# Performance work log

Hardware: AMD Instinct MI355X
Metric: run time of the kernel (lower is better)

## Reference

```python
import jax, jax.numpy as jnp
import numpy as np

B, S, H = 2, 1024, 4096
NH, NKV, HD = 32, 8, 128
THETA = 500000.0
EPS = 1e-6


def _ste(x, q):
    # straight-through estimator: forward q, gradient of identity
    return x + jax.lax.stop_gradient(q - x)


def weight_quant(w):
    # BitNet b1.58 ternary weight quantization (per-tensor mean-abs scale)
    scale = 1.0 / jnp.clip(jnp.mean(jnp.abs(w)), 1e-5)
    wq = jnp.clip(jnp.round(w * scale), -1.0, 1.0) / scale
    return _ste(w, wq)


def act_quant(x):
    # per-token int8 absmax activation quantization
    scale = 127.0 / jnp.clip(jnp.max(jnp.abs(x), axis=-1, keepdims=True), 1e-5)
    xq = jnp.clip(jnp.round(x * scale), -128.0, 127.0) / scale
    return _ste(x, xq)


def bitlinear(x, w):
    # torch Linear convention: w is (out, in)
    return act_quant(x) @ weight_quant(w).T


def rmsnorm(x, w):
    return x * jax.lax.rsqrt(jnp.mean(x * x, axis=-1, keepdims=True) + EPS) * w


def rope(x, cos, sin):
    # x: (b, s, h, hd); pairs are interleaved (even, odd) like view_as_complex
    x2 = x.reshape(*x.shape[:-1], HD // 2, 2)
    a, b = x2[..., 0], x2[..., 1]
    c = cos[None, :, None, :]
    s = sin[None, :, None, :]
    out = jnp.stack([a * c - b * s, a * s + b * c], axis=-1)
    return out.reshape(x.shape)


def setup_inputs() -> dict:
    key = jax.random.key(0)
    ks = jax.random.split(key, 6)
    hidden_states = jax.random.normal(ks[0], (B, S, H), dtype=jnp.float32)
    causal = jnp.tril(jnp.ones((S, S), dtype=bool))
    attention_mask = jnp.where(causal, 0.0, -1e9).astype(jnp.float32)[None, None]
    w_q = jax.random.normal(ks[1], (NH * HD, H), dtype=jnp.float32) * 0.02
    w_k = jax.random.normal(ks[2], (NKV * HD, H), dtype=jnp.float32) * 0.02
    w_v = jax.random.normal(ks[3], (NKV * HD, H), dtype=jnp.float32) * 0.02
    w_o = jax.random.normal(ks[4], (H, NH * HD), dtype=jnp.float32) * 0.02
    subln_w = jnp.ones((NH * HD,), dtype=jnp.float32)
    return {"hidden_states": hidden_states, "attention_mask": attention_mask,
            "w_q": w_q, "w_k": w_k, "w_v": w_v, "w_o": w_o, "subln_w": subln_w}


def reference(hidden_states, attention_mask, w_q, w_k, w_v, w_o, subln_w):
    b, s, _ = hidden_states.shape
    # RoPE tables (precomputed buffer in torch, constant here)
    inv_freq = 1.0 / (THETA ** (jnp.arange(0, HD, 2, dtype=jnp.float32) / HD))
    freqs = jnp.arange(s, dtype=jnp.float32)[:, None] * inv_freq[None, :]  # (s, hd/2)
    cos, sin = jnp.cos(freqs), jnp.sin(freqs)

    q = bitlinear(hidden_states, w_q).reshape(b, s, NH, HD)
    k = bitlinear(hidden_states, w_k).reshape(b, s, NKV, HD)
    v = bitlinear(hidden_states, w_v).reshape(b, s, NKV, HD)

    q = rope(q, cos, sin)
    k = rope(k, cos, sin)

    # GQA: repeat kv heads
    n_rep = NH // NKV
    k = jnp.repeat(k, n_rep, axis=2)  # (b, s, NH, hd)
    v = jnp.repeat(v, n_rep, axis=2)

    scale = 1.0 / np.sqrt(HD)
    scores = jnp.einsum('bqhd,bkhd->bhqk', q, k) * scale
    scores = scores + attention_mask
    attn = jax.nn.softmax(scores.astype(jnp.float32), axis=-1).astype(q.dtype)
    out = jnp.einsum('bhqk,bkhd->bqhd', attn, v).reshape(b, s, NH * HD)

    out = rmsnorm(out, subln_w)  # SubLN before output projection
    out = bitlinear(out, w_o)
    return out
```

## Files before the change

kernel.cpp:

```cpp
#include <hip/hip_runtime.h>
#include <hip/hip_bf16.h>
#include <cstdint>

typedef unsigned short u16;
typedef __bf16 bf16x8 __attribute__((ext_vector_type(8)));
typedef float f32x4 __attribute__((ext_vector_type(4)));
typedef int i32x4 __attribute__((ext_vector_type(4)));

#define SEQ 1024
#define HID 4096
#define NHQ 32
#define NKVH 8
#define HDIM 128
#define NB 2
#define NROWS (NB*SEQ)

static __device__ __forceinline__ u16 f2bf(float x) {
  __hip_bfloat16 h = __float2bfloat16(x);
  return *reinterpret_cast<u16*>(&h);
}

static __device__ __forceinline__ void gload16(const void* g, void* l) {
  __builtin_amdgcn_global_load_lds((__attribute__((address_space(1))) void*)(void*)g,
                                   (__attribute__((address_space(3))) void*)l, 16, 0, 0);
}

static __device__ __forceinline__ int pack4i8(float a, float b, float c, float d,
                                              float s, float lo, float hi) {
  int x0 = (int)fminf(fmaxf(rintf(a*s), lo), hi);
  int x1 = (int)fminf(fmaxf(rintf(b*s), lo), hi);
  int x2 = (int)fminf(fmaxf(rintf(c*s), lo), hi);
  int x3 = (int)fminf(fmaxf(rintf(d*s), lo), hi);
  return (x0 & 255) | ((x1 & 255) << 8) | ((x2 & 255) << 16) | ((x3 & 255) << 24);
}

__global__ __launch_bounds__(256) void k_abssum4(const float* __restrict__ wq_, const float* __restrict__ wk_,
                                                 const float* __restrict__ wv_, const float* __restrict__ wo_,
                                                 float* __restrict__ partial) {
  int bx = blockIdx.x;
  const float* w; long n4; int pbase, lb, nb;
  if (bx < 1024)      { w = wq_; n4 = 4194304; pbase = 0;    lb = bx;        nb = 1024; }
  else if (bx < 1280) { w = wk_; n4 = 1048576; pbase = 1024; lb = bx - 1024; nb = 256; }
  else if (bx < 1536) { w = wv_; n4 = 1048576; pbase = 1280; lb = bx - 1280; nb = 256; }
  else                { w = wo_; n4 = 4194304; pbase = 1536; lb = bx - 1536; nb = 1024; }
  float s = 0.f;
  long stride = (long)nb * 256;
  const float4* w4 = (const float4*)w;
  for (long j = (long)lb*256 + threadIdx.x; j < n4; j += stride) {
    float4 v = w4[j];
    s += fabsf(v.x) + fabsf(v.y) + fabsf(v.z) + fabsf(v.w);
  }
  #pragma unroll
  for (int off = 1; off < 64; off <<= 1) s += __shfl_xor(s, off);
  __shared__ float red[4];
  if ((threadIdx.x & 63) == 0) red[threadIdx.x >> 6] = s;
  __syncthreads();
  if (threadIdx.x == 0) partial[pbase + lb] = red[0] + red[1] + red[2] + red[3];
}

__global__ __launch_bounds__(256) void k_wscale(const float* __restrict__ partial,
                                                float* __restrict__ wsc) {
  __shared__ float red[4];
  const float nelem[4] = {16777216.f, 4194304.f, 4194304.f, 16777216.f};
  const int pbase[4] = {0, 1024, 1280, 1536};
  const int pcnt[4]  = {1024, 256, 256, 1024};
  for (int wi = 0; wi < 4; ++wi) {
    float s = 0.f;
    for (int j = threadIdx.x; j < pcnt[wi]; j += 256) s += partial[pbase[wi] + j];
    #pragma unroll
    for (int off = 1; off < 64; off <<= 1) s += __shfl_xor(s, off);
    if ((threadIdx.x & 63) == 0) red[threadIdx.x >> 6] = s;
    __syncthreads();
    if (threadIdx.x == 0) wsc[wi] = fmaxf((red[0]+red[1]+red[2]+red[3]) / nelem[wi], 1e-5f);
    __syncthreads();
  }
}

__global__ __launch_bounds__(256) void k_quantw8_all(const float* __restrict__ wq_, const float* __restrict__ wk_,
                                                     const float* __restrict__ wv_, const float* __restrict__ wo_,
                                                     char* __restrict__ oq_, char* __restrict__ ok_,
                                                     char* __restrict__ ov_, char* __restrict__ oo_,
                                                     const float* __restrict__ wsc) {
  int bx = blockIdx.x;
  const float* src; char* dst; int idx; long base;
  if (bx < 16384)      { src = wq_; dst = oq_; idx = 0; base = bx; }
  else if (bx < 20480) { src = wk_; dst = ok_; idx = 1; base = bx - 16384; }
  else if (bx < 24576) { src = wv_; dst = ov_; idx = 2; base = bx - 20480; }
  else                 { src = wo_; dst = oo_; idx = 3; base = bx - 24576; }
  long j = base*256 + threadIdx.x;
  long oj = j;
  if (idx <= 1) {
    long row = j >> 10;
    int u = (int)(row & 31);
    long prow = (row & ~31L) | (long)((u >> 1) | ((u & 1) << 4));
    oj = (prow << 10) | (j & 1023);
  }
  float inv = 1.0f / wsc[idx];
  float4 v = ((const float4*)src)[j];
  ((int*)dst)[oj] = pack4i8(v.x, v.y, v.z, v.w, inv, -1.f, 1.f);
}

__global__ __launch_bounds__(256) void k_actq8(const float* __restrict__ x, char* __restrict__ xq,
                                               float* __restrict__ xs) {
  long row = blockIdx.x;
  const float4* xr = (const float4*)(x + row*HID);
  float4 v[4];
  float am = 0.f;
  #pragma unroll
  for (int j = 0; j < 4; ++j) {
    v[j] = xr[j*256 + threadIdx.x];
    am = fmaxf(am, fmaxf(fmaxf(fabsf(v[j].x), fabsf(v[j].y)), fmaxf(fabsf(v[j].z), fabsf(v[j].w))));
  }
  #pragma unroll
  for (int off = 1; off < 64; off <<= 1) am = fmaxf(am, __shfl_xor(am, off));
  __shared__ float red[4];
  if ((threadIdx.x & 63) == 0) red[threadIdx.x >> 6] = am;
  __syncthreads();
  am = fmaxf(fmaxf(red[0], red[1]), fmaxf(red[2], red[3]));
  float amc = fmaxf(am, 1e-5f);
  float s = 127.0f / amc;
  int* oq = (int*)(xq + row*HID);
  #pragma unroll
  for (int j = 0; j < 4; ++j)
    oq[j*256 + threadIdx.x] = pack4i8(v[j].x, v[j].y, v[j].z, v[j].w, s, -128.f, 127.f);
  if (threadIdx.x == 0) xs[row] = amc / 127.0f;
}

__global__ __launch_bounds__(256, 4) void k_gemm8(const char* __restrict__ A, const char* __restrict__ W,
                                                  float* __restrict__ C, const float* __restrict__ arow,
                                                  const float* __restrict__ wsc, int widx,
                                                  int M, int N, int K) {
  __shared__ char As[2][64*64] __attribute__((aligned(16)));
  __shared__ char Ws_[2][128*64] __attribute__((aligned(16)));
  int t = threadIdx.x;
  int l = (blockIdx.x & 7) * 128 + (blockIdx.x >> 3);
  int bn = l >> 5, bm = l & 31;
  const char* Ab = A + (long)bm*64*K;
  const char* Wb = W + (long)bn*128*K;
  int lane = t & 63, wid = t >> 6;
  int wr = wid >> 1, wc = wid & 1;
  int lrow = lane & 15, l8 = lane >> 4;
  int xsw = (lrow >> 1) & 3;
  int ch0 = (l8 ^ xsw) * 16;
  i32x4 zero = {0, 0, 0, 0};
  i32x4 acc[2][4];
  #pragma unroll
  for (int mi = 0; mi < 2; ++mi)
    #pragma unroll
    for (int ni = 0; ni < 4; ++ni) acc[mi][ni] = zero;

  int r0 = t >> 2;
  int c0 = ((t & 3) ^ ((t >> 3) & 3)) * 16;
  auto stage = [&](int buf, int kt) {
    gload16(Ab + (long)r0*K + kt*64 + c0, &As[buf][t*16]);
    gload16(Wb + (long)r0*K + kt*64 + c0, &Ws_[buf][t*16]);
    gload16(Wb + (long)(r0+64)*K + kt*64 + c0, &Ws_[buf][(t+256)*16]);
  };

  int nk = K >> 6;
  stage(0, 0);
  __syncthreads();
  int cur = 0;
  for (int kt = 0; kt < nk; ++kt) {
    if (kt + 1 < nk) stage(cur ^ 1, kt + 1);
    i32x4 af[2], bfr[4];
    #pragma unroll
    for (int mi = 0; mi < 2; ++mi) af[mi] = *(const i32x4*)&As[cur][(wr*32 + mi*16 + lrow)*64 + ch0];
    #pragma unroll
    for (int ni = 0; ni < 4; ++ni) bfr[ni] = *(const i32x4*)&Ws_[cur][(wc*64 + ni*16 + lrow)*64 + ch0];
    __builtin_amdgcn_s_setprio(1);
    #pragma unroll
    for (int mi = 0; mi < 2; ++mi)
      #pragma unroll
      for (int ni = 0; ni < 4; ++ni)
        acc[mi][ni] = __builtin_amdgcn_mfma_i32_16x16x64_i8(af[mi], bfr[ni], acc[mi][ni], 0, 0, 0);
    __builtin_amdgcn_s_setprio(0);
    __syncthreads();
    cur ^= 1;
  }
  float ws = wsc[widx];
  #pragma unroll
  for (int mi = 0; mi < 2; ++mi)
    #pragma unroll
    for (int r = 0; r < 4; ++r) {
      int row = bm*64 + wr*32 + mi*16 + l8*4 + r;
      float sc = arow[row] * ws;
      #pragma unroll
      for (int ni = 0; ni < 4; ++ni) {
        int col = bn*128 + wc*64 + ni*16 + lrow;
        C[(long)row*N + col] = (float)acc[mi][ni][r] * sc;
      }
    }
}

__global__ __launch_bounds__(256) void k_gemm8_qkv(const char* __restrict__ A,
    const char* __restrict__ Wq, const char* __restrict__ Wk, const char* __restrict__ Wv,
    u16* __restrict__ Qb, u16* __restrict__ Kb, u16* __restrict__ Vt,
    const float* __restrict__ arow, const float* __restrict__ wsc,
    const float* __restrict__ cosb, const float* __restrict__ sinb) {
  const int K = 4096;
  int bx = (blockIdx.x & 7) * 96 + (blockIdx.x >> 3);
  int kind, bm, bn;
  const char* W;
  if (bx < 512)      { kind = 0; bm = bx >> 5;          bn = bx & 31; W = Wq; }
  else if (bx < 640) { kind = 1; bm = (bx - 512) >> 3;  bn = bx & 7;  W = Wk; }
  else               { kind = 2; bm = (bx - 640) >> 3;  bn = bx & 7;  W = Wv; }

  __shared__ char As[2][128*64] __attribute__((aligned(16)));
  __shared__ char Ws_[2][128*64] __attribute__((aligned(16)));
  int t = threadIdx.x;
  const char* Ab = A + (long)bm*128*K;
  const char* Wb = W + (long)bn*128*K;
  int lane = t & 63, wid = t >> 6;
  int wr = wid >> 1, wc = wid & 1;
  int lrow = lane & 15, l8 = lane >> 4;
  int xsw = (lrow >> 1) & 3;
  int ch0 = (l8 ^ xsw) * 16;
  i32x4 zero = {0, 0, 0, 0};
  i32x4 acc[4][4];
  #pragma unroll
  for (int mi = 0; mi < 4; ++mi)
    #pragma unroll
    for (int ni = 0; ni < 4; ++ni) acc[mi][ni] = zero;

  int f0 = t, f1 = t + 256;
  int r0 = f0 >> 2, c0 = ((f0 & 3) ^ ((f0 >> 3) & 3)) * 16;
  int r1 = f1 >> 2;
  auto stage = [&](int buf, int kt) {
    gload16(Ab + (long)r0*K + kt*64 + c0, &As[buf][f0*16]);
    gload16(Ab + (long)r1*K + kt*64 + c0, &As[buf][f1*16]);
    gload16(Wb + (long)r0*K + kt*64 + c0, &Ws_[buf][f0*16]);
    gload16(Wb + (long)r1*K + kt*64 + c0, &Ws_[buf][f1*16]);
  };

  stage(0, 0);
  __syncthreads();
  int cur = 0;
  for (int kt = 0; kt < (K >> 6); ++kt) {
    if (kt + 1 < (K >> 6)) stage(cur ^ 1, kt + 1);
    i32x4 af[4], bfr[4];
    #pragma unroll
    for (int mi = 0; mi < 4; ++mi) af[mi] = *(const i32x4*)&As[cur][(wr*64 + mi*16 + lrow)*64 + ch0];
    #pragma unroll
    for (int ni = 0; ni < 4; ++ni) bfr[ni] = *(const i32x4*)&Ws_[cur][(wc*64 + ni*16 + lrow)*64 + ch0];
    __builtin_amdgcn_s_setprio(1);
    #pragma unroll
    for (int mi = 0; mi < 4; ++mi)
      #pragma unroll
      for (int ni = 0; ni < 4; ++ni)
        acc[mi][ni] = __builtin_amdgcn_mfma_i32_16x16x64_i8(af[mi], bfr[ni], acc[mi][ni], 0, 0, 0);
    __builtin_amdgcn_s_setprio(0);
    __syncthreads();
    cur ^= 1;
  }

  if (kind == 2) {
    float ws = wsc[2];
    #pragma unroll
    for (int mi = 0; mi < 4; ++mi) {
      int row0 = bm*128 + wr*64 + mi*16 + l8*4;
      int bidx = row0 >> 10, s0 = row0 & 1023;
      #pragma unroll
      for (int ni = 0; ni < 4; ++ni) {
        int col = bn*128 + wc*64 + ni*16 + lrow;
        int hkv = col >> 7, d = col & 127;
        ushort4 o4;
        o4.x = f2bf((float)acc[mi][ni][0] * arow[row0+0] * ws);
        o4.y = f2bf((float)acc[mi][ni][1] * arow[row0+1] * ws);
        o4.z = f2bf((float)acc[mi][ni][2] * arow[row0+2] * ws);
        o4.w = f2bf((float)acc[mi][ni][3] * arow[row0+3] * ws);
        *(ushort4*)&Vt[(((long)bidx*NKVH + hkv)*HDIM + d)*SEQ + s0] = o4;
      }
    }
  } else {
    float ws = wsc[kind];
    u16* dst = kind ? Kb : Qb;
    int nh = kind ? NKVH : NHQ;
    #pragma unroll
    for (int mi = 0; mi < 4; ++mi) {
      #pragma unroll
      for (int r = 0; r < 4; ++r) {
        int row = bm*128 + wr*64 + mi*16 + l8*4 + r;
        int bidx = row >> 10, s = row & 1023;
        float sc = arow[row] * ws;
        #pragma unroll
        for (int j = 0; j < 2; ++j) {
          float a  = (float)acc[mi][2*j][r] * sc;
          float b2 = (float)acc[mi][2*j+1][r] * sc;
          int B = bn*128 + wc*64 + j*32;
          int h = B >> 7;
          int d = (B & 127) + 2*lrow;
          int i = d >> 1;
          float cc = cosb[(s << 6) + i], sn = sinb[(s << 6) + i];
          ushort2 o2;
          o2.x = f2bf(a*cc - b2*sn);
          o2.y = f2bf(a*sn + b2*cc);
          *(ushort2*)&dst[(((long)bidx*nh + h)*SEQ + s)*HDIM + d] = o2;
        }
      }
    }
  }
}

__global__ __launch_bounds__(256) void k_ropetab(float* __restrict__ cosb, float* __restrict__ sinb) {
  int idx = blockIdx.x*256 + threadIdx.x;
  int s = idx >> 6, i = idx & 63;
  float e = (2.0f * (float)i) / 128.0f;
  float inv = 1.0f / powf(500000.0f, e);
  float f = (float)s * inv;
  cosb[idx] = cosf(f);
  sinb[idx] = sinf(f);
}

__global__ __launch_bounds__(256) void k_attn(const u16* __restrict__ qb, const u16* __restrict__ kb,
                                              const u16* __restrict__ vt, float* __restrict__ ao) {
  int p = blockIdx.x, h = blockIdx.y, b = blockIdx.z;
  int t = threadIdx.x, lane = t & 63, wid = t >> 6;
  int lrow = lane & 15, l8 = lane >> 4;
  int x7 = lrow & 7;

  __shared__ u16 Ks[2][64*128] __attribute__((aligned(16)));
  __shared__ u16 Vs[2][128*64] __attribute__((aligned(16)));
  __shared__ u16 Ps[4][16][72] __attribute__((aligned(16)));

  const u16* kp = kb + ((long)(b*NKVH + (h >> 2)))*SEQ*HDIM;
  const u16* vp = vt + ((long)(b*NKVH + (h >> 2)))*HDIM*SEQ;

  auto stageK = [&](int buf, int j) {
    const u16* src = kp + (long)j*64*HDIM;
    #pragma unroll
    for (int i = 0; i < 4; ++i) {
      int r0 = wid*16 + i*4;
      int row = r0 + (lane >> 4);
      int cg = (lane & 15) ^ (row & 7);
      gload16(src + (long)row*HDIM + cg*8, &Ks[buf][r0*HDIM]);
    }
  };
  auto stageV = [&](int buf, int j) {
    #pragma unroll
    for (int i = 0; i < 4; ++i) {
      int r0 = wid*32 + i*8;
      int row = r0 + (lane >> 3);
      int cg = (lane & 7) ^ (row & 7);
      gload16(vp + (long)row*SEQ + j*64 + cg*8, &Vs[buf][r0*64]);
    }
  };

  for (int phase = 0; phase < 2; ++phase) {
    int qt = phase ? (15 - p) : p;
    int q0 = qt*64 + wid*16;
    const u16* qp = qb + (((long)(b*NHQ + h))*SEQ + q0)*HDIM;
    bf16x8 qf[4];
    #pragma unroll
    for (int ks = 0; ks < 4; ++ks) qf[ks] = *(const bf16x8*)&qp[lrow*HDIM + ks*32 + l8*8];
    f32x4 zero = {0.f, 0.f, 0.f, 0.f};
    f32x4 o[8];
    #pragma unroll
    for (int f = 0; f < 8; ++f) o[f] = zero;
    float m[4], ll[4];
    #pragma unroll
    for (int r = 0; r < 4; ++r) { m[r] = -1e30f; ll[r] = 0.f; }

    int nj = qt + 1;
    stageK(0, 0); stageV(0, 0);
    __syncthreads();
    int cur = 0;
    for (int j = 0; j < nj; ++j) {
      if (j + 1 < nj) { stageK(cur ^ 1, j + 1); stageV(cur ^ 1, j + 1); }
      const u16* Kc = Ks[cur];
      const u16* Vc = Vs[cur];
      f32x4 sc4[4];
      #pragma unroll
      for (int ni = 0; ni < 4; ++ni) sc4[ni] = zero;
      __builtin_amdgcn_s_setprio(1);
      #pragma unroll
      for (int ni = 0; ni < 4; ++ni) {
        int row = ni*16 + lrow;
        #pragma unroll
        for (int ks = 0; ks < 4; ++ks) {
          int cl = (ks*4 + l8) ^ x7;
          bf16x8 kfr = *(const bf16x8*)&Kc[row*HDIM + cl*8];
          sc4[ni] = __builtin_amdgcn_mfma_f32_16x16x32_bf16(qf[ks], kfr, sc4[ni], 0, 0, 0);
        }
      }
      __builtin_amdgcn_s_setprio(0);
      const float scale = 0.08838834764831845f;
      float pm[4] = {-1e30f, -1e30f, -1e30f, -1e30f};
      float pv[4][4];
      bool diag = (j == qt);
      #pragma unroll
      for (int ni = 0; ni < 4; ++ni) {
        int kv = j*64 + ni*16 + lrow;
        #pragma unroll
        for (int r = 0; r < 4; ++r) {
          int qr = q0 + l8*4 + r;
          float val = sc4[ni][r] * scale;
          if (diag && kv > qr) val = -1e30f;
          pv[ni][r] = val;
          pm[r] = fmaxf(pm[r], val);
        }
      }
      #pragma unroll
      for (int r = 0; r < 4; ++r) {
        #pragma unroll
        for (int off = 1; off < 16; off <<= 1) pm[r] = fmaxf(pm[r], __shfl_xor(pm[r], off));
      }
      float fr[4], rs[4];
      #pragma unroll
      for (int r = 0; r < 4; ++r) {
        float nm = fmaxf(m[r], pm[r]);
        fr[r] = __expf(m[r] - nm);
        m[r] = nm; rs[r] = 0.f;
      }
      #pragma unroll
      for (int ni = 0; ni < 4; ++ni)
        #pragma unroll
        for (int r = 0; r < 4; ++r) {
          float pe = __expf(pv[ni][r] - m[r]);
          pv[ni][r] = pe; rs[r] += pe;
        }
      #pragma unroll
      for (int r = 0; r < 4; ++r) {
        #pragma unroll
        for (int off = 1; off < 16; off <<= 1) rs[r] += __shfl_xor(rs[r], off);
        ll[r] = ll[r]*fr[r] + rs[r];
      }
      #pragma unroll
      for (int f = 0; f < 8; ++f) {
        o[f][0] *= fr[0]; o[f][1] *= fr[1]; o[f][2] *= fr[2]; o[f][3] *= fr[3];
      }
      #pragma unroll
      for (int ni = 0; ni < 4; ++ni)
        #pragma unroll
        for (int r = 0; r < 4; ++r)
          Ps[wid][l8*4 + r][ni*16 + lrow] = f2bf(pv[ni][r]);
      bf16x8 pf0 = *(const bf16x8*)&Ps[wid][lrow][l8*8];
      bf16x8 pf1 = *(const bf16x8*)&Ps[wid][lrow][32 + l8*8];
      __builtin_amdgcn_s_setprio(1);
      #pragma unroll
      for (int f = 0; f < 8; ++f) {
        int d = f*16 + lrow;
        bf16x8 v0 = *(const bf16x8*)&Vc[d*64 + ((l8) ^ x7)*8];
        bf16x8 v1 = *(const bf16x8*)&Vc[d*64 + ((4 + l8) ^ x7)*8];
        o[f] = __builtin_amdgcn_mfma_f32_16x16x32_bf16(pf0, v0, o[f], 0, 0, 0);
        o[f] = __builtin_amdgcn_mfma_f32_16x16x32_bf16(pf1, v1, o[f], 0, 0, 0);
      }
      __builtin_amdgcn_s_setprio(0);
      __syncthreads();
      cur ^= 1;
    }
    float invl[4];
    #pragma unroll
    for (int r = 0; r < 4; ++r) invl[r] = 1.0f / ll[r];
    #pragma unroll
    for (int f = 0; f < 8; ++f)
      #pragma unroll
      for (int r = 0; r < 4; ++r) {
        long row = (long)b*SEQ + q0 + l8*4 + r;
        ao[row*HID + h*HDIM + f*16 + lrow] = o[f][r] * invl[r];
      }
    __syncthreads();
  }
}

__global__ __launch_bounds__(256) void k_rmsq8(const float* __restrict__ x, const float* __restrict__ w,
                                               char* __restrict__ yq, float* __restrict__ ys) {
  long row = blockIdx.x;
  const float4* xr = (const float4*)(x + row*HID);
  const float4* wr = (const float4*)w;
  float4 v[4];
  float ss = 0.f;
  #pragma unroll
  for (int j = 0; j < 4; ++j) {
    v[j] = xr[j*256 + threadIdx.x];
    ss += v[j].x*v[j].x + v[j].y*v[j].y + v[j].z*v[j].z + v[j].w*v[j].w;
  }
  #pragma unroll
  for (int off = 1; off < 64; off <<= 1) ss += __shfl_xor(ss, off);
  __shared__ float red[4];
  if ((threadIdx.x & 63) == 0) red[threadIdx.x >> 6] = ss;
  __syncthreads();
  ss = red[0] + red[1] + red[2] + red[3];
  __syncthreads();
  float rn = rsqrtf(ss / (float)HID + 1e-6f);
  float4 y[4];
  float am = 0.f;
  #pragma unroll
  for (int j = 0; j < 4; ++j) {
    float4 wv = wr[j*256 + threadIdx.x];
    y[j].x = v[j].x * rn * wv.x; y[j].y = v[j].y * rn * wv.y;
    y[j].z = v[j].z * rn * wv.z; y[j].w = v[j].w * rn * wv.w;
    am = fmaxf(am, fmaxf(fmaxf(fabsf(y[j].x), fabsf(y[j].y)), fmaxf(fabsf(y[j].z), fabsf(y[j].w))));
  }
  #pragma unroll
  for (int off = 1; off < 64; off <<= 1) am = fmaxf(am, __shfl_xor(am, off));
  if ((threadIdx.x & 63) == 0) red[threadIdx.x >> 6] = am;
  __syncthreads();
  am = fmaxf(fmaxf(red[0], red[1]), fmaxf(red[2], red[3]));
  float amc = fmaxf(am, 1e-5f);
  float s = 127.0f / amc;
  int* oq = (int*)(yq + row*HID);
  #pragma unroll
  for (int j = 0; j < 4; ++j)
    oq[j*256 + threadIdx.x] = pack4i8(y[j].x, y[j].y, y[j].z, y[j].w, s, -128.f, 127.f);
  if (threadIdx.x == 0) ys[row] = amc / 127.0f;
}

extern "C" void kernel_launch(void* const* d_in, const int* in_sizes, int n_in,
                              void* d_out, int out_size, void* d_ws, size_t ws_size,
                              hipStream_t stream) {
  const float* hs    = (const float*)d_in[0];
  const float* w_q   = (const float*)d_in[2];
  const float* w_k   = (const float*)d_in[3];
  const float* w_v   = (const float*)d_in[4];
  const float* w_o   = (const float*)d_in[5];
  const float* subln = (const float*)d_in[6];

  char* ws = (char*)d_ws;
  char*  wqq = (char*)(ws + 0L);
  char*  wqk = (char*)(ws + 16777216L);
  char*  wqv = (char*)(ws + 20971520L);
  char*  wqo = (char*)(ws + 25165824L);
  char*  xq  = (char*)(ws + 41943040L);
  float* ao  = (float*)(ws + 50331648L);
  char*  yq  = (char*)(ws + 83886080L);
  u16*   qb  = (u16*)(ws + 92274688L);
  u16*   kb  = (u16*)(ws + 109051904L);
  u16*   vtb = (u16*)(ws + 113246208L);
  float* cosb= (float*)(ws + 117440512L);
  float* sinb= (float*)(ws + 117702656L);
  float* xs  = (float*)(ws + 117964800L);
  float* ys  = (float*)(ws + 117972992L);
  float* wsc = (float*)(ws + 117981184L);
  float* par = (float*)(ws + 117981248L);
  float* out = (float*)d_out;

  k_abssum4<<<2560, 256, 0, stream>>>(w_q, w_k, w_v, w_o, par);
  k_wscale<<<1, 256, 0, stream>>>(par, wsc);

  k_quantw8_all<<<40960, 256, 0, stream>>>(w_q, w_k, w_v, w_o, wqq, wqk, wqv, wqo, wsc);
  k_ropetab<<<256, 256, 0, stream>>>(cosb, sinb);
  k_actq8<<<NROWS, 256, 0, stream>>>(hs, xq, xs);

  k_gemm8_qkv<<<768, 256, 0, stream>>>(xq, wqq, wqk, wqv, qb, kb, vtb, xs, wsc, cosb, sinb);

  k_attn<<<dim3(8, 32, 2), 256, 0, stream>>>(qb, kb, vtb, ao);

  k_rmsq8<<<NROWS, 256, 0, stream>>>(ao, subln, yq, ys);

  k_gemm8<<<1024, 256, 0, stream>>>(yq, wqo, out, ys, wsc, 3, NROWS, 4096, 4096);
}
```

Measured before the change: 297.2 us.

## Triple-buffer int8 GEMM tiles with explicit vmcnt waits and XCD-aware block mapping

Both int8 GEMM kernels move from double to triple buffering of LDS tiles. They prefetch two k-steps ahead and use explicit s_waitcnt vmcnt counts plus raw s_barrier instead of __syncthreads, which keeps more global loads in flight. The block-to-tile mapping is also changed so each XCD gets a compact 2D block of output tiles, improving L2 reuse of A and W. The cost is more LDS per block, which lowers occupancy; the o-proj kernel also drops its launch-bounds occupancy hint.

```diff
diff --git a/kernel.cpp b/kernel.cpp
--- a/kernel.cpp
+++ b/kernel.cpp
@@ -126,15 +126,17 @@
   if (threadIdx.x == 0) xs[row] = amc / 127.0f;
 }
 
-__global__ __launch_bounds__(256, 4) void k_gemm8(const char* __restrict__ A, const char* __restrict__ W,
-                                                  float* __restrict__ C, const float* __restrict__ arow,
-                                                  const float* __restrict__ wsc, int widx,
-                                                  int M, int N, int K) {
-  __shared__ char As[2][64*64] __attribute__((aligned(16)));
-  __shared__ char Ws_[2][128*64] __attribute__((aligned(16)));
+__global__ __launch_bounds__(256) void k_gemm8(const char* __restrict__ A, const char* __restrict__ W,
+                                               float* __restrict__ C, const float* __restrict__ arow,
+                                               const float* __restrict__ wsc, int widx,
+                                               int M, int N, int K) {
+  __shared__ char As[3][64*64] __attribute__((aligned(16)));
+  __shared__ char Ws_[3][128*64] __attribute__((aligned(16)));
   int t = threadIdx.x;
-  int l = (blockIdx.x & 7) * 128 + (blockIdx.x >> 3);
-  int bn = l >> 5, bm = l & 31;
+  int bid = blockIdx.x;
+  int xcd = bid & 7, w = bid >> 3;
+  int bm = ((xcd & 1) << 4) + (w >> 3);
+  int bn = ((xcd >> 1) << 3) + (w & 7);
   const char* Ab = A + (long)bm*64*K;
   const char* Wb = W + (long)bn*128*K;
   int lane = t & 63, wid = t >> 6;
@@ -158,16 +160,26 @@
   };
 
   int nk = K >> 6;
-  stage(0, 0);
-  __syncthreads();
-  int cur = 0;
+  stage(0, 0); stage(1, 1);
   for (int kt = 0; kt < nk; ++kt) {
-    if (kt + 1 < nk) stage(cur ^ 1, kt + 1);
+    if (kt + 2 < nk) {
+      stage((kt + 2) % 3, kt + 2);
+      asm volatile("s_waitcnt vmcnt(6)" ::: "memory");
+    } else if (kt + 1 < nk) {
+      asm volatile("s_waitcnt vmcnt(3)" ::: "memory");
+    } else {
+      asm volatile("s_waitcnt vmcnt(0)" ::: "memory");
+    }
+    __builtin_amdgcn_sched_barrier(0);
+    __builtin_amdgcn_s_barrier();
+    int cur = kt % 3;
+    const char* Ac = &As[cur][0];
+    const char* Wc = &Ws_[cur][0];
     i32x4 af[2], bfr[4];
     #pragma unroll
-    for (int mi = 0; mi < 2; ++mi) af[mi] = *(const i32x4*)&As[cur][(wr*32 + mi*16 + lrow)*64 + ch0];
-    #pragma unroll
-    for (int ni = 0; ni < 4; ++ni) bfr[ni] = *(const i32x4*)&Ws_[cur][(wc*64 + ni*16 + lrow)*64 + ch0];
+    for (int mi = 0; mi < 2; ++mi) af[mi] = *(const i32x4*)&Ac[(wr*32 + mi*16 + lrow)*64 + ch0];
+    #pragma unroll
+    for (int ni = 0; ni < 4; ++ni) bfr[ni] = *(const i32x4*)&Wc[(wc*64 + ni*16 + lrow)*64 + ch0];
     __builtin_amdgcn_s_setprio(1);
     #pragma unroll
     for (int mi = 0; mi < 2; ++mi)
@@ -175,8 +187,9 @@
       for (int ni = 0; ni < 4; ++ni)
         acc[mi][ni] = __builtin_amdgcn_mfma_i32_16x16x64_i8(af[mi], bfr[ni], acc[mi][ni], 0, 0, 0);
     __builtin_amdgcn_s_setprio(0);
-    __syncthreads();
-    cur ^= 1;
+    asm volatile("s_waitcnt lgkmcnt(0)" ::: "memory");
+    __builtin_amdgcn_sched_barrier(0);
+    __builtin_amdgcn_s_barrier();
   }
   float ws = wsc[widx];
   #pragma unroll
@@ -199,15 +212,16 @@
     const float* __restrict__ arow, const float* __restrict__ wsc,
     const float* __restrict__ cosb, const float* __restrict__ sinb) {
   const int K = 4096;
-  int bx = (blockIdx.x & 7) * 96 + (blockIdx.x >> 3);
+  int bid = blockIdx.x;
+  int xcd = bid & 7, w = bid >> 3;
   int kind, bm, bn;
   const char* W;
-  if (bx < 512)      { kind = 0; bm = bx >> 5;          bn = bx & 31; W = Wq; }
-  else if (bx < 640) { kind = 1; bm = (bx - 512) >> 3;  bn = bx & 7;  W = Wk; }
-  else               { kind = 2; bm = (bx - 640) >> 3;  bn = bx & 7;  W = Wv; }
-
-  __shared__ char As[2][128*64] __attribute__((aligned(16)));
-  __shared__ char Ws_[2][128*64] __attribute__((aligned(16)));
+  if (w < 64)      { kind = 0; bm = ((xcd & 1) << 3) + (w >> 3); bn = ((xcd >> 1) << 3) + (w & 7); W = Wq; }
+  else if (w < 80) { int u = w - 64; kind = 1; bm = (xcd << 1) + (u >> 3); bn = u & 7; W = Wk; }
+  else             { int u = w - 80; kind = 2; bm = (xcd << 1) + (u >> 3); bn = u & 7; W = Wv; }
+
+  __shared__ char As[3][128*64] __attribute__((aligned(16)));
+  __shared__ char Ws_[3][128*64] __attribute__((aligned(16)));
   int t = threadIdx.x;
   const char* Ab = A + (long)bm*128*K;
   const char* Wb = W + (long)bn*128*K;
@@ -233,16 +247,27 @@
     gload16(Wb + (long)r1*K + kt*64 + c0, &Ws_[buf][f1*16]);
   };
 
-  stage(0, 0);
-  __syncthreads();
-  int cur = 0;
-  for (int kt = 0; kt < (K >> 6); ++kt) {
-    if (kt + 1 < (K >> 6)) stage(cur ^ 1, kt + 1);
+  int nk = K >> 6;
+  stage(0, 0); stage(1, 1);
+  for (int kt = 0; kt < nk; ++kt) {
+    if (kt + 2 < nk) {
+      stage((kt + 2) % 3, kt + 2);
+      asm volatile("s_waitcnt vmcnt(8)" ::: "memory");
+    } else if (kt + 1 < nk) {
+      asm volatile("s_waitcnt vmcnt(4)" ::: "memory");
+    } else {
+      asm volatile("s_waitcnt vmcnt(0)" ::: "memory");
+    }
+    __builtin_amdgcn_sched_barrier(0);
+    __builtin_amdgcn_s_barrier();
+    int cur = kt % 3;
+    const char* Ac = &As[cur][0];
+    const char* Wc = &Ws_[cur][0];
     i32x4 af[4], bfr[4];
     #pragma unroll
-    for (int mi = 0; mi < 4; ++mi) af[mi] = *(const i32x4*)&As[cur][(wr*64 + mi*16 + lrow)*64 + ch0];
-    #pragma unroll
-    for (int ni = 0; ni < 4; ++ni) bfr[ni] = *(const i32x4*)&Ws_[cur][(wc*64 + ni*16 + lrow)*64 + ch0];
+    for (int mi = 0; mi < 4; ++mi) af[mi] = *(const i32x4*)&Ac[(wr*64 + mi*16 + lrow)*64 + ch0];
+    #pragma unroll
+    for (int ni = 0; ni < 4; ++ni) bfr[ni] = *(const i32x4*)&Wc[(wc*64 + ni*16 + lrow)*64 + ch0];
     __builtin_amdgcn_s_setprio(1);
     #pragma unroll
     for (int mi = 0; mi < 4; ++mi)
@@ -250,8 +275,9 @@
       for (int ni = 0; ni < 4; ++ni)
         acc[mi][ni] = __builtin_amdgcn_mfma_i32_16x16x64_i8(af[mi], bfr[ni], acc[mi][ni], 0, 0, 0);
     __builtin_amdgcn_s_setprio(0);
-    __syncthreads();
-    cur ^= 1;
+    asm volatile("s_waitcnt lgkmcnt(0)" ::: "memory");
+    __builtin_amdgcn_sched_barrier(0);
+    __builtin_amdgcn_s_barrier();
   }
 
   if (kind == 2) {
```

Result: faster. 277.0 us (-6.8%).
